# Performance work log

Hardware: AMD Instinct MI355X
Metric: run time of the kernel (lower is better)

## Reference

```python
import jax, jax.numpy as jnp
import numpy as np

VOLRADIUS = 64.0
DT = 1.0 / VOLRADIUS          # normalized step size (dt / volradius)
NSTEPS = 64                   # covers t in [0, 1.0) at step DT


def setup_inputs() -> dict:
    key = jax.random.key(0)
    ks = jax.random.split(key, 8)
    B, H, W, K, M = 1, 128, 128, 32, 16
    # ray origins near volume center, unit directions
    raypos = 0.2 * jax.random.normal(ks[0], (B, H, W, 3), jnp.float32)
    rd = jax.random.normal(ks[1], (B, H, W, 3), jnp.float32)
    raydir = rd / jnp.linalg.norm(rd, axis=-1, keepdims=True)
    tmin = jnp.zeros((B, H, W), jnp.float32)
    tmax = 0.9 + 0.1 * jax.random.uniform(ks[2], (B, H, W), dtype=jnp.float32)
    tminmax = jnp.stack([tmin, tmax], axis=-1)
    # primitive poses: positions, rotations (orthonormal via QR), inverse-scales
    primpos = 0.3 * jax.random.normal(ks[3], (B, K, 3), jnp.float32)
    A = jax.random.normal(ks[4], (B, K, 3, 3), jnp.float32)
    primrot, _ = jnp.linalg.qr(A)
    primscale = 1.0 + 2.0 * jax.random.uniform(ks[5], (B, K, 3), dtype=jnp.float32)
    # RGBA voxel payload per primitive; alpha channel nonnegative (decoder emits nonneg density)
    template = jax.random.normal(ks[6], (B, K, 4, M, M, M), jnp.float32)
    template = template.at[:, :, 3].set(2.0 * jax.nn.softplus(template[:, :, 3]))
    return dict(raypos=raypos, raydir=raydir, tminmax=tminmax, primpos=primpos,
                primrot=primrot, primscale=primscale, template=template)


def _trilinear(template, y):
    # template [B,K,C,M,M,M]; y [B,R,K,3] normalized coords in [-1,1] (align_corners)
    B, K, C, M = template.shape[0], template.shape[1], template.shape[2], template.shape[3]
    g = (y + 1.0) * 0.5 * (M - 1)
    i0 = jnp.clip(jnp.floor(g), 0, M - 2).astype(jnp.int32)
    f = jnp.clip(g - i0.astype(g.dtype), 0.0, 1.0)
    i1 = i0 + 1
    bidx = jnp.arange(B)[:, None, None]
    kidx = jnp.arange(K)[None, None, :]

    def corner(iz, iy, ix):
        # advanced-index gather -> [B,R,K,C]
        return template[bidx, kidx, :, iz, iy, ix]

    fz, fy, fx = f[..., 0:1], f[..., 1:2], f[..., 2:3]
    i0z, i0y, i0x = i0[..., 0], i0[..., 1], i0[..., 2]
    i1z, i1y, i1x = i1[..., 0], i1[..., 1], i1[..., 2]
    v = ((1 - fz) * (1 - fy) * (1 - fx) * corner(i0z, i0y, i0x)
         + (1 - fz) * (1 - fy) * fx * corner(i0z, i0y, i1x)
         + (1 - fz) * fy * (1 - fx) * corner(i0z, i1y, i0x)
         + (1 - fz) * fy * fx * corner(i0z, i1y, i1x)
         + fz * (1 - fy) * (1 - fx) * corner(i1z, i0y, i0x)
         + fz * (1 - fy) * fx * corner(i1z, i0y, i1x)
         + fz * fy * (1 - fx) * corner(i1z, i1y, i0x)
         + fz * fy * fx * corner(i1z, i1y, i1x))
    return v  # [B,R,K,C]


def reference(raypos, raydir, tminmax, primpos, primrot, primscale, template):
    B, H, W, _ = raypos.shape
    R = H * W
    rp = raypos.reshape(B, R, 3)
    rd = raydir.reshape(B, R, 3)
    tmm = tminmax.reshape(B, R, 2)
    tmin, tmax = tmm[..., 0:1], tmm[..., 1:2]

    def step(carry, i):
        rgb, alpha = carry
        t = tmin + i * DT                                   # [B,R,1]
        pos = rp + rd * t                                   # [B,R,3]
        xl = pos[:, :, None, :] - primpos[:, None, :, :]    # [B,R,K,3]
        yloc = jnp.einsum('bkij,brkj->brki', primrot, xl) * primscale[:, None, :, :]
        inside = jnp.all(jnp.abs(yloc) <= 1.0, axis=-1, keepdims=True).astype(rgb.dtype)
        samp = (_trilinear(template, yloc) * inside).sum(axis=2)   # [B,R,4]
        srgb, salpha = samp[..., :3], samp[..., 3:4]
        valid = (t < tmax).astype(rgb.dtype)
        # clamped additive compositing (Neural Volumes / MVP)
        newalpha = jnp.clip(alpha + salpha * DT * valid, 0.0, 1.0)
        contrib = newalpha - alpha
        return (rgb + srgb * contrib, newalpha), None

    init = (jnp.zeros((B, R, 3), raypos.dtype), jnp.zeros((B, R, 1), raypos.dtype))
    (rgb, alpha), _ = jax.lax.scan(step, init, jnp.arange(NSTEPS, dtype=raypos.dtype))

    rayrgba = jnp.concatenate([rgb, alpha], axis=-1).reshape(B, H, W, 4)
    rayrgba = jnp.transpose(rayrgba, (0, 3, 1, 2))   # [B,4,H,W]
    rayrgb = rayrgba[:, :3]
    rayalpha = rayrgba[:, 3:4]
    return rayrgb, rayalpha, rayrgba
```

## Files before the change

kernel.cpp:

```cpp
#include <hip/hip_runtime.h>
#include <hip/hip_fp16.h>


namespace {

constexpr float kDT  = 1.0f / 64.0f;
constexpr int   kVox = 32 * 4096;

struct H4 { __half2 lo, hi; };
struct __attribute__((aligned(8))) H4x2 { __half2 l0, h0, l1, h1; };

__global__ __launch_bounds__(256) void transpose_tmpl_h(
    const float* __restrict__ tmpl, H4* __restrict__ wsH)
{
    const int idx = blockIdx.x * 256 + threadIdx.x;
    const int k   = idx >> 12;
    const int rem = idx & 4095;
    const float* src = tmpl + k * 16384 + rem;
    H4 v;
    v.lo = __floats2half2_rn(src[0],    src[4096]);
    v.hi = __floats2half2_rn(src[8192], src[12288]);
    wsH[idx] = v;
}

__device__ __forceinline__ __half2 lerp2(__half2 a, __half2 b, __half2 f) {
    return __hfma2(f, __hsub2(b, a), a);
}

template<int CTRL>
__device__ __forceinline__ float dpp_add(float v) {
    return v + __int_as_float(__builtin_amdgcn_update_dpp(
        0, __float_as_int(v), CTRL, 0xF, 0xF, true));
}

__device__ __forceinline__ float half_sum32(float v) {
    v = dpp_add<0xB1>(v);
    v = dpp_add<0x4E>(v);
    v = dpp_add<0x141>(v);
    v = dpp_add<0x140>(v);
    v += __int_as_float(__builtin_amdgcn_ds_swizzle(__float_as_int(v), 0x401F));
    return v;
}

__global__ __launch_bounds__(128) void raymarch14(
    const float* __restrict__ raypos,
    const float* __restrict__ raydir,
    const float* __restrict__ tminmax,
    const float* __restrict__ primpos,
    const float* __restrict__ primrot,
    const float* __restrict__ primscale,
    const H4* __restrict__ wsH,
    float* __restrict__ out,
    int R)
{
    const int lane   = threadIdx.x & 63;
    const int wid    = threadIdx.x >> 6;
    const int k      = lane & 31;
    const int parity = lane >> 5;
    const int ray    = blockIdx.x * 2 + wid;

    const float rpx = raypos[ray * 3 + 0];
    const float rpy = raypos[ray * 3 + 1];
    const float rpz = raypos[ray * 3 + 2];
    const float rdx = raydir[ray * 3 + 0];
    const float rdy = raydir[ray * 3 + 1];
    const float rdz = raydir[ray * 3 + 2];
    const float tmin = tminmax[ray * 2 + 0];
    const float tmax = tminmax[ray * 2 + 1];

    float A0, A1, A2, D0, D1, D2;
    {
        const float ox = rpx - primpos[k * 3 + 0];
        const float oy = rpy - primpos[k * 3 + 1];
        const float oz = rpz - primpos[k * 3 + 2];
        const float s0 = primscale[k * 3 + 0];
        const float s1 = primscale[k * 3 + 1];
        const float s2 = primscale[k * 3 + 2];
        const float* rk = primrot + k * 9;
        A0 = (rk[0] * ox + rk[1] * oy + rk[2] * oz) * s0;
        D0 = (rk[0] * rdx + rk[1] * rdy + rk[2] * rdz) * s0;
        A1 = (rk[3] * ox + rk[4] * oy + rk[5] * oz) * s1;
        D1 = (rk[3] * rdx + rk[4] * rdy + rk[5] * rdz) * s1;
        A2 = (rk[6] * ox + rk[7] * oy + rk[8] * oz) * s2;
        D2 = (rk[6] * rdx + rk[7] * rdy + rk[8] * rdz) * s2;
    }

    const H4* __restrict__ tbase = wsH + k * 4096;

    float alpha = 0.f;
    float r0 = 0.f, r1 = 0.f, r2 = 0.f;

#define COORDS(SUB, IN, AD, FZ, FY, FX)                                  \
    {                                                                    \
        const float tl = fmaf((float)(SUB), kDT, tmin);                  \
        const float y0 = fmaf(D0, tl, A0);                               \
        const float y1 = fmaf(D1, tl, A1);                               \
        const float y2 = fmaf(D2, tl, A2);                               \
        IN = (tl < tmax) && fabsf(y0) <= 1.0f                            \
           && fabsf(y1) <= 1.0f && fabsf(y2) <= 1.0f;                    \
        const float gz = fmaf(y0, 7.5f, 7.5f);                           \
        const float gy = fmaf(y1, 7.5f, 7.5f);                           \
        const float gx = fmaf(y2, 7.5f, 7.5f);                           \
        const int iz = min((int)gz, 14);                                 \
        const int iy = min((int)gy, 14);                                 \
        const int ix = min((int)gx, 14);                                 \
        FZ = fminf(gz - (float)iz, 1.0f);                                \
        FY = fminf(gy - (float)iy, 1.0f);                                \
        FX = fminf(gx - (float)ix, 1.0f);                                \
        AD = iz * 256 + iy * 16 + ix;                                    \
    }

#define EVAL(IN, AD, FZ, FY, FX, S0, S1, S2, S3)                         \
    {                                                                    \
        S0 = 0.f; S1 = 0.f; S2 = 0.f; S3 = 0.f;                         \
        if (IN) {                                                        \
            const H4* tp = tbase + (AD);                                 \
            const H4x2 p00 = *(const H4x2*)(tp + 0);                     \
            const H4x2 p01 = *(const H4x2*)(tp + 16);                    \
            const H4x2 p10 = *(const H4x2*)(tp + 256);                   \
            const H4x2 p11 = *(const H4x2*)(tp + 272);                   \
            const __half2 hz = __float2half2_rn(FZ);                     \
            const __half2 hy = __float2half2_rn(FY);                     \
            const __half2 hx = __float2half2_rn(FX);                     \
            const __half2 q0l0 = lerp2(p00.l0, p10.l0, hz);              \
            const __half2 q0h0 = lerp2(p00.h0, p10.h0, hz);              \
            const __half2 q0l1 = lerp2(p00.l1, p10.l1, hz);              \
            const __half2 q0h1 = lerp2(p00.h1, p10.h1, hz);              \
            const __half2 q1l0 = lerp2(p01.l0, p11.l0, hz);              \
            const __half2 q1h0 = lerp2(p01.h0, p11.h0, hz);              \
            const __half2 q1l1 = lerp2(p01.l1, p11.l1, hz);              \
            const __half2 q1h1 = lerp2(p01.h1, p11.h1, hz);              \
            const __half2 ul0 = lerp2(q0l0, q1l0, hy);                   \
            const __half2 uh0 = lerp2(q0h0, q1h0, hy);                   \
            const __half2 ul1 = lerp2(q0l1, q1l1, hy);                   \
            const __half2 uh1 = lerp2(q0h1, q1h1, hy);                   \
            const __half2 vl = lerp2(ul0, ul1, hx);                      \
            const __half2 vh = lerp2(uh0, uh1, hx);                      \
            const float2 fLo = __half22float2(vl);                       \
            const float2 fHi = __half22float2(vh);                       \
            S0 = fLo.x; S1 = fLo.y; S2 = fHi.x; S3 = fHi.y;              \
        }                                                                \
    }

    for (int j = 0; j < 16; ++j) {
        bool  inA, inB;
        int   adA, adB;
        float fzA, fyA, fxA, fzB, fyB, fxB;
        COORDS(4 * j + parity,     inA, adA, fzA, fyA, fxA);
        COORDS(4 * j + 2 + parity, inB, adB, fzB, fyB, fxB);

        if (__ballot(inA || inB)) {
            float s0a, s1a, s2a, s3a, s0b, s1b, s2b, s3b;
            EVAL(inA, adA, fzA, fyA, fxA, s0a, s1a, s2a, s3a);
            EVAL(inB, adB, fzB, fyB, fxB, s0b, s1b, s2b, s3b);

            const float ta = half_sum32(s3a);
            const float tb = half_sum32(s3b);
            const float sum2 = ta + tb;
            const float tot4 = sum2 + __shfl_xor(sum2, 32);
            const float anew = fmaf(tot4, kDT, alpha);

            float ca, cb;
            if (anew < 1.0f) {
                ca = ta * kDT;
                cb = tb * kDT;
                alpha = anew;
            } else {
                const float oa = __shfl_xor(ta, 32);
                const float ob = __shfl_xor(tb, 32);
                const float te0 = parity ? oa : ta;
                const float to0 = parity ? ta : oa;
                const float te1 = parity ? ob : tb;
                const float to1 = parity ? tb : ob;
                const float a1 = fminf(fmaf(te0, kDT, alpha), 1.0f);
                const float c0 = a1 - alpha;
                const float a2 = fminf(fmaf(to0, kDT, a1), 1.0f);
                const float c1 = a2 - a1;
                const float a3 = fminf(fmaf(te1, kDT, a2), 1.0f);
                const float c2 = a3 - a2;
                const float a4 = fminf(fmaf(to1, kDT, a3), 1.0f);
                const float c3 = a4 - a3;
                alpha = a4;
                ca = parity ? c1 : c0;
                cb = parity ? c3 : c2;
            }

            r0 = fmaf(s0a, ca, fmaf(s0b, cb, r0));
            r1 = fmaf(s1a, ca, fmaf(s1b, cb, r1));
            r2 = fmaf(s2a, ca, fmaf(s2b, cb, r2));
        }

        const float tn = fmaf((float)(4 * j + 4), kDT, tmin);
        if (tn >= tmax || alpha >= 1.0f) break;
    }

#undef COORDS
#undef EVAL

    r0 = half_sum32(r0); r0 += __shfl_xor(r0, 32);
    r1 = half_sum32(r1); r1 += __shfl_xor(r1, 32);
    r2 = half_sum32(r2); r2 += __shfl_xor(r2, 32);

    if (lane == 0) {
        out[0 * R + ray] = r0;
        out[1 * R + ray] = r1;
        out[2 * R + ray] = r2;
        out[3 * R + ray] = alpha;
        out[4 * R + ray] = r0;
        out[5 * R + ray] = r1;
        out[6 * R + ray] = r2;
        out[7 * R + ray] = alpha;
    }
}

__global__ __launch_bounds__(256) void raymarch_fb(
    const float* __restrict__ raypos, const float* __restrict__ raydir,
    const float* __restrict__ tminmax, const float* __restrict__ primpos,
    const float* __restrict__ primrot, const float* __restrict__ primscale,
    const float* __restrict__ tmpl, float* __restrict__ out, int R)
{
    const int lane = threadIdx.x & 63;
    const int wid  = threadIdx.x >> 6;
    const int k    = lane & 31;
    const int half = lane >> 5;
    const int ray  = blockIdx.x * 8 + wid * 2 + half;

    const float rpx = raypos[ray*3+0], rpy = raypos[ray*3+1], rpz = raypos[ray*3+2];
    const float rdx = raydir[ray*3+0], rdy = raydir[ray*3+1], rdz = raydir[ray*3+2];
    const float tmin = tminmax[ray*2+0], tmax = tminmax[ray*2+1];

    float A0,A1,A2,D0,D1,D2;
    {
        const float ox = rpx - primpos[k*3+0], oy = rpy - primpos[k*3+1], oz = rpz - primpos[k*3+2];
        const float s0 = primscale[k*3+0], s1 = primscale[k*3+1], s2 = primscale[k*3+2];
        const float* rk = primrot + k*9;
        A0 = (rk[0]*ox+rk[1]*oy+rk[2]*oz)*s0; D0 = (rk[0]*rdx+rk[1]*rdy+rk[2]*rdz)*s0;
        A1 = (rk[3]*ox+rk[4]*oy+rk[5]*oz)*s1; D1 = (rk[3]*rdx+rk[4]*rdy+rk[5]*rdz)*s1;
        A2 = (rk[6]*ox+rk[7]*oy+rk[8]*oz)*s2; D2 = (rk[6]*rdx+rk[7]*rdy+rk[8]*rdz)*s2;
    }
    float alpha = 0.f, r0 = 0.f, r1 = 0.f, r2 = 0.f;
    for (int i = 0; i < 64; ++i) {
        const float t = fmaf((float)i, kDT, tmin);
        const bool live = (t < tmax) && (alpha < 1.0f);
        if (__ballot(live) == 0ull) break;
        const float y0 = fmaf(D0,t,A0), y1 = fmaf(D1,t,A1), y2 = fmaf(D2,t,A2);
        const bool inside = live && fabsf(y0)<=1.f && fabsf(y1)<=1.f && fabsf(y2)<=1.f;
        if (__ballot(inside) == 0ull) continue;
        float s0=0.f,s1=0.f,s2=0.f,s3=0.f;
        if (inside) {
            const float gz=(y0+1.f)*7.5f, gy=(y1+1.f)*7.5f, gx=(y2+1.f)*7.5f;
            const int iz=(int)fminf(floorf(gz),14.f), iy=(int)fminf(floorf(gy),14.f), ix=(int)fminf(floorf(gx),14.f);
            const float fz=fminf(gz-(float)iz,1.f), fy=fminf(gy-(float)iy,1.f), fx=fminf(gx-(float)ix,1.f);
            const float oz_=1.f-fz, oy_=1.f-fy, ox_=1.f-fx;
            const float w000=oz_*oy_*ox_, w001=oz_*oy_*fx, w010=oz_*fy*ox_, w011=oz_*fy*fx;
            const float w100=fz*oy_*ox_, w101=fz*oy_*fx, w110=fz*fy*ox_, w111=fz*fy*fx;
            const float* tp = tmpl + k*16384 + iz*256 + iy*16 + ix;
            float acc[4];
            #pragma unroll
            for (int c = 0; c < 4; ++c) {
                const float* tc = tp + c*4096;
                acc[c] = w000*tc[0]+w001*tc[1]+w010*tc[16]+w011*tc[17]
                       + w100*tc[256]+w101*tc[257]+w110*tc[272]+w111*tc[273];
            }
            s0=acc[0]; s1=acc[1]; s2=acc[2]; s3=acc[3];
        }
        float tot3 = s3;
        #pragma unroll
        for (int m = 1; m < 32; m <<= 1) tot3 += __shfl_xor(tot3, m);
        const float na = fminf(fmaf(tot3, kDT, alpha), 1.0f);
        const float contrib = na - alpha;
        alpha = na;
        r0 = fmaf(s0, contrib, r0); r1 = fmaf(s1, contrib, r1); r2 = fmaf(s2, contrib, r2);
    }
    #pragma unroll
    for (int m = 1; m < 32; m <<= 1) {
        r0 += __shfl_xor(r0, m); r1 += __shfl_xor(r1, m); r2 += __shfl_xor(r2, m);
    }
    if (k == 0) {
        out[0*R+ray]=r0; out[1*R+ray]=r1; out[2*R+ray]=r2; out[3*R+ray]=alpha;
        out[4*R+ray]=r0; out[5*R+ray]=r1; out[6*R+ray]=r2; out[7*R+ray]=alpha;
    }
}

}

extern "C" void kernel_launch(void* const* d_in, const int* in_sizes, int n_in,
                              void* d_out, int out_size, void* d_ws, size_t ws_size,
                              hipStream_t stream) {
    const float* raypos    = (const float*)d_in[0];
    const float* raydir    = (const float*)d_in[1];
    const float* tminmax   = (const float*)d_in[2];
    const float* primpos   = (const float*)d_in[3];
    const float* primrot   = (const float*)d_in[4];
    const float* primscale = (const float*)d_in[5];
    const float* tmpl      = (const float*)d_in[6];
    float* out = (float*)d_out;

    const int R = in_sizes[0] / 3;
    const size_t needH = (size_t)kVox * sizeof(H4);

    if (ws_size >= needH) {
        H4* wsH = (H4*)d_ws;
        transpose_tmpl_h<<<dim3(kVox / 256), dim3(256), 0, stream>>>(tmpl, wsH);
        raymarch14<<<dim3(R / 2), dim3(128), 0, stream>>>(
            raypos, raydir, tminmax, primpos, primrot, primscale, wsH, out, R);
    } else {
        raymarch_fb<<<dim3(R / 8), dim3(256), 0, stream>>>(
            raypos, raydir, tminmax, primpos, primrot, primscale, tmpl, out, R);
    }
}
```

Before: 86.26 us.

## Pre-expand template into per-cell 8-corner blocks for contiguous trilinear fetches

```diff
diff --git a/kernel.cpp b/kernel.cpp
--- a/kernel.cpp
+++ b/kernel.cpp
@@ -5,22 +5,37 @@
 namespace {
 
 constexpr float kDT  = 1.0f / 64.0f;
-constexpr int   kVox = 32 * 4096;
+constexpr int   kCells = 32 * 4096;
 
 struct H4 { __half2 lo, hi; };
 struct __attribute__((aligned(8))) H4x2 { __half2 l0, h0, l1, h1; };
 
-__global__ __launch_bounds__(256) void transpose_tmpl_h(
-    const float* __restrict__ tmpl, H4* __restrict__ wsH)
+__global__ __launch_bounds__(256) void build_cells(
+    const float* __restrict__ tmpl, H4* __restrict__ wsC)
 {
     const int idx = blockIdx.x * 256 + threadIdx.x;
     const int k   = idx >> 12;
     const int rem = idx & 4095;
-    const float* src = tmpl + k * 16384 + rem;
-    H4 v;
-    v.lo = __floats2half2_rn(src[0],    src[4096]);
-    v.hi = __floats2half2_rn(src[8192], src[12288]);
-    wsH[idx] = v;
+    const int iz  = rem >> 8;
+    const int iy  = (rem >> 4) & 15;
+    const int ix  = rem & 15;
+    const float* base = tmpl + k * 16384;
+
+    H4 cell[8];
+    #pragma unroll
+    for (int d = 0; d < 8; ++d) {
+        const int z = min(iz + (d >> 2), 15);
+        const int y = min(iy + ((d >> 1) & 1), 15);
+        const int x = min(ix + (d & 1), 15);
+        const float* s = base + z * 256 + y * 16 + x;
+        cell[d].lo = __floats2half2_rn(s[0],    s[4096]);
+        cell[d].hi = __floats2half2_rn(s[8192], s[12288]);
+    }
+    H4* dst = wsC + (size_t)idx * 8;
+    *(H4x2*)(dst + 0) = *(H4x2*)&cell[0];
+    *(H4x2*)(dst + 2) = *(H4x2*)&cell[2];
+    *(H4x2*)(dst + 4) = *(H4x2*)&cell[4];
+    *(H4x2*)(dst + 6) = *(H4x2*)&cell[6];
 }
 
 __device__ __forceinline__ __half2 lerp2(__half2 a, __half2 b, __half2 f) {
@@ -42,14 +57,14 @@
     return v;
 }
 
-__global__ __launch_bounds__(128) void raymarch14(
+__global__ __launch_bounds__(128) void raymarch15(
     const float* __restrict__ raypos,
     const float* __restrict__ raydir,
     const float* __restrict__ tminmax,
     const float* __restrict__ primpos,
     const float* __restrict__ primrot,
     const float* __restrict__ primscale,
-    const H4* __restrict__ wsH,
+    const H4* __restrict__ wsC,
     float* __restrict__ out,
     int R)
 {
@@ -85,7 +100,7 @@
         D2 = (rk[6] * rdx + rk[7] * rdy + rk[8] * rdz) * s2;
     }
 
-    const H4* __restrict__ tbase = wsH + k * 4096;
+    const H4* __restrict__ cbase = wsC + ((size_t)k << 15);
 
     float alpha = 0.f;
     float r0 = 0.f, r1 = 0.f, r2 = 0.f;
@@ -114,11 +129,11 @@
     {                                                                    \
         S0 = 0.f; S1 = 0.f; S2 = 0.f; S3 = 0.f;                         \
         if (IN) {                                                        \
-            const H4* tp = tbase + (AD);                                 \
-            const H4x2 p00 = *(const H4x2*)(tp + 0);                     \
-            const H4x2 p01 = *(const H4x2*)(tp + 16);                    \
-            const H4x2 p10 = *(const H4x2*)(tp + 256);                   \
-            const H4x2 p11 = *(const H4x2*)(tp + 272);                   \
+            const H4x2* cp = (const H4x2*)(cbase + ((size_t)(AD) * 8));  \
+            const H4x2 p00 = cp[0];                                      \
+            const H4x2 p01 = cp[1];                                      \
+            const H4x2 p10 = cp[2];                                      \
+            const H4x2 p11 = cp[3];                                      \
             const __half2 hz = __float2half2_rn(FZ);                     \
             const __half2 hy = __float2half2_rn(FY);                     \
             const __half2 hx = __float2half2_rn(FX);                     \
@@ -297,13 +312,13 @@
     float* out = (float*)d_out;
 
     const int R = in_sizes[0] / 3;
-    const size_t needH = (size_t)kVox * sizeof(H4);
-
-    if (ws_size >= needH) {
-        H4* wsH = (H4*)d_ws;
-        transpose_tmpl_h<<<dim3(kVox / 256), dim3(256), 0, stream>>>(tmpl, wsH);
-        raymarch14<<<dim3(R / 2), dim3(128), 0, stream>>>(
-            raypos, raydir, tminmax, primpos, primrot, primscale, wsH, out, R);
+    const size_t needC = (size_t)kCells * 64;
+
+    if (ws_size >= needC) {
+        H4* wsC = (H4*)d_ws;
+        build_cells<<<dim3(kCells / 256), dim3(256), 0, stream>>>(tmpl, wsC);
+        raymarch15<<<dim3(R / 2), dim3(128), 0, stream>>>(
+            raypos, raydir, tminmax, primpos, primrot, primscale, wsC, out, R);
     } else {
         raymarch_fb<<<dim3(R / 8), dim3(256), 0, stream>>>(
             raypos, raydir, tminmax, primpos, primrot, primscale, tmpl, out, R);
```

Result: slower. 89.83 us (+4.1%).
